# Optimization experiments

Hardware: AMD Instinct MI355X
Metric: run time of the kernel (lower is better)

The kernel has to match this reference:

```python
import jax, jax.numpy as jnp
import numpy as np
from math import sqrt

C = 64        # res_channels
LAYERS = 30
CYCLE = 10
T = 1000
B = 16
L = 32768


def setup_inputs() -> dict:
    key = jax.random.key(0)
    ks = jax.random.split(key, 12)

    def p(k, shape):
        return jax.random.normal(k, shape, dtype=jnp.float32) * 0.05

    # DiffusionEmbedding._build_embedding(T+1): table[s, 2d] = cos(s*10^(4d/63)), table[s,2d+1]=sin(...)
    steps = np.arange(T + 1, dtype=np.float64)[:, None]           # [T+1, 1]
    ang = steps * 10.0 ** (np.arange(64)[None, :] * 4.0 / 63.0)   # [T+1, 64]
    emb_table = jnp.asarray(
        np.stack([np.cos(ang), np.sin(ang)], axis=-1).reshape(T + 1, 128),
        dtype=jnp.float32,
    )

    return {
        "audio": jax.random.normal(ks[0], (B, L), dtype=jnp.float32),
        "diffusion_step": jax.random.randint(ks[1], (B,), 0, T),
        "emb_table": emb_table,                      # [T+1, 128]
        "W1": p(ks[2], (512, 128)), "b1": jnp.zeros((512,), jnp.float32),
        "W2": p(ks[3], (512, 512)), "b2": jnp.zeros((512,), jnp.float32),
        "Win": p(ks[4], (C,)),      "bin_": jnp.zeros((C,), jnp.float32),   # 1x1 conv 1->C
        "diff_W": p(ks[5], (LAYERS, C, 512)),   "diff_b": jnp.zeros((LAYERS, C), jnp.float32),
        "dconv_W": p(ks[6], (LAYERS, 2 * C, C, 3)), "dconv_b": jnp.zeros((LAYERS, 2 * C), jnp.float32),
        "out_W": p(ks[7], (LAYERS, 2 * C, C)),  "out_b": jnp.zeros((LAYERS, 2 * C), jnp.float32),
        "Wo1": p(ks[8], (C, C)),    "bo1": jnp.zeros((C,), jnp.float32),
        "Wo2": p(ks[9], (1, C)),    "bo2": jnp.zeros((1,), jnp.float32),
    }


def _dilated_conv(x, w, d):
    # x: [B, C, L], w: [2C, C, 3], 'same' padding with dilation d
    return jax.lax.conv_general_dilated(
        x, w, window_strides=(1,), padding=[(d, d)], rhs_dilation=(d,),
        dimension_numbers=("NCH", "OIH", "NCH"))


def reference(audio, diffusion_step, emb_table, W1, b1, W2, b2, Win, bin_,
              diff_W, diff_b, dconv_W, dconv_b, out_W, out_b, Wo1, bo1, Wo2, bo2):
    # input projection: Conv1d(1, C, 1) + ReLU
    x = jax.nn.relu(audio[:, None, :] * Win[None, :, None] + bin_[None, :, None])  # [B, C, L]

    t = emb_table[diffusion_step]                  # [B, 128]
    t = jax.nn.silu(t @ W1.T + b1)                 # [B, 512]
    t = jax.nn.silu(t @ W2.T + b2)                 # [B, 512]

    skip = jnp.zeros_like(x)
    for i in range(LAYERS):
        d = 2 ** (i % CYCLE)
        dp = jnp.einsum("bk,ck->bc", t, diff_W[i]) + diff_b[i]          # [B, C]
        y = _dilated_conv(x + dp[:, :, None], dconv_W[i], d)
        y = y + dconv_b[i][None, :, None]                                # [B, 2C, L]
        y = jnp.tanh(y[:, :C]) * jax.nn.sigmoid(y[:, C:])                # gated activation [B, C, L]
        z = jnp.einsum("oc,bcl->bol", out_W[i], y) + out_b[i][None, :, None]  # [B, 2C, L]
        x = (x + z[:, :C]) / sqrt(2.0)
        skip = skip + z[:, C:]

    h = skip / sqrt(float(LAYERS))
    h = jax.nn.relu(jnp.einsum("oc,bcl->bol", Wo1, h) + bo1[None, :, None])
    out = jnp.einsum("oc,bcl->bol", Wo2, h) + bo2[None, :, None]         # [B, 1, L]
    return out[:, 0, :]                                                  # [B, L]
```

## Files before the change

### kernel.cpp

```cpp
#include <hip/hip_runtime.h>
#include <hip/hip_bf16.h>
#include <math.h>
#include <stdint.h>

#define NLAYERS 30
#define BB 16
#define LL 32768
#define SEG 256
#define NT (SEG / 16)

#define SS 16384.0f
#define SSI (1.0f / 16384.0f)

typedef __attribute__((ext_vector_type(8))) short bf16x8;
typedef __attribute__((ext_vector_type(8))) short s16x8;
typedef __attribute__((ext_vector_type(4))) float f32x4;

__device__ inline float bf2f(ushort u) {
    union { uint i; float f; } v; v.i = ((uint)u) << 16; return v.f;
}
__device__ inline ushort f2bf(float f) {
    uint u = __float_as_uint(f);
    return (ushort)((u + 0x7FFFu + ((u >> 16) & 1u)) >> 16);
}

__global__ void emb_kernel(const int* __restrict__ step, const float* __restrict__ emb,
                           const float* __restrict__ W1, const float* __restrict__ b1,
                           const float* __restrict__ W2, const float* __restrict__ b2,
                           float* __restrict__ t_out) {
    int b = blockIdx.x, j = threadIdx.x;
    __shared__ float e[128];
    __shared__ float t1[512];
    int s = step[b];
    if (j < 128) e[j] = emb[s * 128 + j];
    __syncthreads();
    float acc = b1[j];
    const float* w = W1 + j * 128;
    for (int k = 0; k < 128; ++k) acc += w[k] * e[k];
    t1[j] = acc / (1.f + __expf(-acc));
    __syncthreads();
    float acc2 = b2[j];
    const float* w2 = W2 + j * 512;
    for (int k = 0; k < 512; ++k) acc2 += w2[k] * t1[k];
    t_out[b * 512 + j] = acc2 / (1.f + __expf(-acc2));
}

__global__ void dp_kernel(const float* __restrict__ t, const float* __restrict__ diff_W,
                          const float* __restrict__ diff_b, float* __restrict__ dp) {
    int i = blockIdx.x, b = blockIdx.y, c = threadIdx.x;
    __shared__ float ts[512];
    for (int k = c; k < 512; k += 64) ts[k] = t[b * 512 + k];
    __syncthreads();
    const float* w = diff_W + (size_t)(i * 64 + c) * 512;
    float acc = diff_b[i * 64 + c];
    for (int k = 0; k < 512; ++k) acc += w[k] * ts[k];
    dp[(i * BB + b) * 64 + c] = acc;
}

__global__ void prep_w_kernel(const float* __restrict__ dconv_W, ushort* __restrict__ wB,
                              const float* __restrict__ out_W, ushort* __restrict__ oB,
                              const float* __restrict__ Wo1, ushort* __restrict__ Wo1B) {
    int idx = blockIdx.x * 256 + threadIdx.x;
    if (idx < 30 * 8 * 6 * 512) {
        int i = idx / 24576;
        int r = idx % 24576;
        int mt = r / 3072;
        int s = (r / 512) % 6;
        int lane = (r >> 3) & 63;
        int j = r & 7;
        int o = mt * 16 + (lane & 15);
        int tap = s >> 1;
        int c = (s & 1) * 32 + (lane >> 4) * 8 + j;
        wB[idx] = f2bf(dconv_W[((size_t)(i * 128 + o) * 64 + c) * 3 + tap]);
    }
    if (idx < 30 * 8 * 2 * 512) {
        int i = idx / 8192;
        int r = idx % 8192;
        int mt = r / 1024;
        int s = (r / 512) % 2;
        int lane = (r >> 3) & 63;
        int j = r & 7;
        int o = mt * 16 + (lane & 15);
        int c = s * 32 + (lane >> 4) * 8 + j;
        oB[idx] = f2bf(out_W[(size_t)(i * 128 + o) * 64 + c]);
    }
    if (idx < 4 * 2 * 512) {
        int mt = idx / 1024;
        int s = (idx / 512) % 2;
        int lane = (idx >> 3) & 63;
        int j = idx & 7;
        int o = mt * 16 + (lane & 15);
        int c = s * 32 + (lane >> 4) * 8 + j;
        const float hscale = SSI * 0.18257418583505537115f;
        Wo1B[idx] = f2bf(Wo1[o * 64 + c] * hscale);
    }
}

__global__ void bias3_kernel(const float* __restrict__ dp, const float* __restrict__ dconv_W,
                             const float* __restrict__ dconv_b, float* __restrict__ bias3) {
    int i = blockIdx.x, b = blockIdx.y, o = threadIdx.x;
    __shared__ float sdp[64];
    if (o < 64) sdp[o] = dp[(i * BB + b) * 64 + o];
    __syncthreads();
    const float* wrow = dconv_W + (size_t)(i * 128 + o) * 192;
    float f = 0.f, lft = 0.f, rgt = 0.f;
    for (int c = 0; c < 64; ++c) {
        float w0 = wrow[c * 3 + 0], w1 = wrow[c * 3 + 1], w2 = wrow[c * 3 + 2];
        float dv = sdp[c];
        f += dv * (w0 + w1 + w2);
        lft += dv * w0;
        rgt += dv * w2;
    }
    float* dst = bias3 + (size_t)(i * BB + b) * 384;
    dst[o] = f + dconv_b[i * 128 + o];
    dst[128 + o] = lft;
    dst[256 + o] = rgt;
}

__global__ void inproj_kernel(const float* __restrict__ audio, const float* __restrict__ Win,
                              const float* __restrict__ bin_, ushort* __restrict__ x) {
    int idx = blockIdx.x * 256 + threadIdx.x;
    int c8 = idx & 7;
    int l = (idx >> 3) & (LL - 1);
    int b = idx >> 18;
    float a = audio[(size_t)b * LL + l];
    ushort us[8];
    #pragma unroll
    for (int cc = 0; cc < 8; ++cc) {
        int c = c8 * 8 + cc;
        float v = a * Win[c] + bin_[c];
        us[cc] = f2bf(v > 0.f ? v : 0.f);
    }
    ushort4* dst = (ushort4*)(x + ((size_t)b * LL + l) * 64 + c8 * 8);
    dst[0] = make_ushort4(us[0], us[1], us[2], us[3]);
    dst[1] = make_ushort4(us[4], us[5], us[6], us[7]);
}

__global__ __launch_bounds__(256) void layer_fused(
    const ushort* __restrict__ xin, ushort* __restrict__ xout, int16_t* __restrict__ skip,
    const ushort* __restrict__ wB,
    const ushort* __restrict__ oB,
    const float* __restrict__ bias3,
    const float* __restrict__ out_b,
    int d) {
    __shared__ __align__(16) ushort su[2][16][72];

    const int b = blockIdx.y;
    const int seg = blockIdx.x;
    const int tid = threadIdx.x;
    const int lane = tid & 63;
    const int p = tid >> 6;
    const int n = lane & 15;
    const int kg = lane >> 4;
    const int rlo = p * 16 + kg * 4;

    bf16x8 A0[6], A1[6], P0[2], P1[2];
    #pragma unroll
    for (int s = 0; s < 6; ++s) {
        A0[s] = *(const bf16x8*)(wB + ((size_t)(p * 6 + s) * 64 + lane) * 8);
        A1[s] = *(const bf16x8*)(wB + ((size_t)((p + 4) * 6 + s) * 64 + lane) * 8);
    }
    #pragma unroll
    for (int s = 0; s < 2; ++s) {
        P0[s] = *(const bf16x8*)(oB + ((size_t)(p * 2 + s) * 64 + lane) * 8);
        P1[s] = *(const bf16x8*)(oB + ((size_t)((p + 4) * 2 + s) * 64 + lane) * 8);
    }
    const float* bb = bias3 + (size_t)b * 384;
    f32x4 bF_lo = *(const f32x4*)(bb + rlo);
    f32x4 bF_hi = *(const f32x4*)(bb + 64 + rlo);
    f32x4 bL_lo = *(const f32x4*)(bb + 128 + rlo);
    f32x4 bL_hi = *(const f32x4*)(bb + 192 + rlo);
    f32x4 bR_lo = *(const f32x4*)(bb + 256 + rlo);
    f32x4 bR_hi = *(const f32x4*)(bb + 320 + rlo);
    f32x4 obL = *(const f32x4*)(out_b + rlo);
    f32x4 obH = *(const f32x4*)(out_b + 64 + rlo);

    const ushort* xb = xin + (size_t)b * LL * 64;
    ushort* xo = xout + (size_t)b * LL * 64;
    int16_t* sb = skip + (size_t)b * LL * 64;
    const float inv_s2 = 0.70710678118654752440f;

#define LOADB(DST, TT)                                                           \
    {                                                                            \
        const int l0_ = seg * SEG + (TT) * 16;                                   \
        _Pragma("unroll")                                                        \
        for (int tap = 0; tap < 3; ++tap) {                                      \
            int lx = l0_ + n + (tap - 1) * d;                                    \
            bool v = (lx >= 0) && (lx < LL);                                     \
            _Pragma("unroll")                                                    \
            for (int h = 0; h < 2; ++h) {                                        \
                bf16x8 bv = {0, 0, 0, 0, 0, 0, 0, 0};                            \
                if (v) bv = *(const bf16x8*)(xb + (size_t)lx * 64 + h * 32 + kg * 8); \
                DST[tap * 2 + h] = bv;                                           \
            }                                                                    \
        }                                                                        \
    }

#define LOADE(XV, SO, TT)                                                        \
    {                                                                            \
        size_t off_ = (size_t)(seg * SEG + (TT) * 16 + n) * 64 + rlo;            \
        XV = *(const ushort4*)(xb + off_);                                       \
        SO = *(const short4*)(sb + off_);                                        \
    }

#define BODY(TT, BUF, BF, XV, SO)                                                \
    {                                                                            \
        f32x4 accL = {0.f, 0.f, 0.f, 0.f}, accH = {0.f, 0.f, 0.f, 0.f};          \
        _Pragma("unroll")                                                        \
        for (int s = 0; s < 6; ++s) {                                            \
            accL = __builtin_amdgcn_mfma_f32_16x16x32_bf16(A0[s], BF[s], accL, 0, 0, 0); \
            accH = __builtin_amdgcn_mfma_f32_16x16x32_bf16(A1[s], BF[s], accH, 0, 0, 0); \
        }                                                                        \
        const int lx0 = seg * SEG + (TT) * 16 + n;                               \
        float selL = (lx0 < d) ? 1.f : 0.f;                                      \
        float selR = (lx0 >= LL - d) ? 1.f : 0.f;                                \
        ushort4 uq;                                                              \
        _Pragma("unroll")                                                        \
        for (int j = 0; j < 4; ++j) {                                            \
            float lo = accL[j] + bF_lo[j] - selL * bL_lo[j] - selR * bR_lo[j];   \
            float hi = accH[j] + bF_hi[j] - selL * bL_hi[j] - selR * bR_hi[j];   \
            float tv = 1.f - 2.f / (1.f + __expf(2.f * lo));                     \
            float sv = 1.f / (1.f + __expf(-hi));                                \
            ushort q = f2bf(tv * sv);                                            \
            if (j == 0) uq.x = q;                                                \
            if (j == 1) uq.y = q;                                                \
            if (j == 2) uq.z = q;                                                \
            if (j == 3) uq.w = q;                                                \
        }                                                                        \
        *(ushort4*)&su[BUF][n][rlo] = uq;                                        \
        asm volatile("s_waitcnt lgkmcnt(0)" ::: "memory");                       \
        __builtin_amdgcn_s_barrier();                                            \
        asm volatile("" ::: "memory");                                           \
        bf16x8 Bp0 = *(const bf16x8*)&su[BUF][n][kg * 8];                        \
        bf16x8 Bp1 = *(const bf16x8*)&su[BUF][n][32 + kg * 8];                   \
        f32x4 zL = {0.f, 0.f, 0.f, 0.f}, zH = {0.f, 0.f, 0.f, 0.f};              \
        zL = __builtin_amdgcn_mfma_f32_16x16x32_bf16(P0[0], Bp0, zL, 0, 0, 0);   \
        zH = __builtin_amdgcn_mfma_f32_16x16x32_bf16(P1[0], Bp0, zH, 0, 0, 0);   \
        zL = __builtin_amdgcn_mfma_f32_16x16x32_bf16(P0[1], Bp1, zL, 0, 0, 0);   \
        zH = __builtin_amdgcn_mfma_f32_16x16x32_bf16(P1[1], Bp1, zH, 0, 0, 0);   \
        size_t off = (size_t)lx0 * 64 + rlo;                                     \
        ushort4 xn;                                                              \
        xn.x = f2bf((bf2f(XV.x) + zL[0] + obL[0]) * inv_s2);                     \
        xn.y = f2bf((bf2f(XV.y) + zL[1] + obL[1]) * inv_s2);                     \
        xn.z = f2bf((bf2f(XV.z) + zL[2] + obL[2]) * inv_s2);                     \
        xn.w = f2bf((bf2f(XV.w) + zL[3] + obL[3]) * inv_s2);                     \
        *(ushort4*)(xo + off) = xn;                                              \
        short4 sn;                                                               \
        float v;                                                                 \
        v = fminf(fmaxf((float)SO.x * SSI + zH[0] + obH[0], -1.999f), 1.999f);   \
        sn.x = (short)__float2int_rn(v * SS);                                    \
        v = fminf(fmaxf((float)SO.y * SSI + zH[1] + obH[1], -1.999f), 1.999f);   \
        sn.y = (short)__float2int_rn(v * SS);                                    \
        v = fminf(fmaxf((float)SO.z * SSI + zH[2] + obH[2], -1.999f), 1.999f);   \
        sn.z = (short)__float2int_rn(v * SS);                                    \
        v = fminf(fmaxf((float)SO.w * SSI + zH[3] + obH[3], -1.999f), 1.999f);   \
        sn.w = (short)__float2int_rn(v * SS);                                    \
        *(short4*)(sb + off) = sn;                                               \
    }

    bf16x8 FA[6], FB[6];
    ushort4 xvA, xvB;
    short4 soA, soB;
    LOADB(FA, 0)
    LOADE(xvA, soA, 0)
    for (int t = 0; t < NT; t += 2) {
        LOADB(FB, t + 1)
        LOADE(xvB, soB, t + 1)
        BODY(t, 0, FA, xvA, soA)
        const int tn = (t + 2 < NT) ? t + 2 : NT - 2;
        LOADB(FA, tn)
        LOADE(xvA, soA, tn)
        BODY(t + 1, 1, FB, xvB, soB)
    }
#undef LOADB
#undef LOADE
#undef BODY
}

__global__ __launch_bounds__(256) void head_mfma(const int16_t* __restrict__ skip,
                                                 const ushort* __restrict__ Wo1B,
                                                 const float* __restrict__ bo1,
                                                 const float* __restrict__ Wo2,
                                                 const float* __restrict__ bo2,
                                                 float* __restrict__ out) {
    const int b = blockIdx.y;
    const int seg = blockIdx.x;
    const int tid = threadIdx.x;
    const int lane = tid & 63;
    const int w = tid >> 6;
    const int n = lane & 15;
    const int kg = lane >> 4;

    bf16x8 A[4][2];
    #pragma unroll
    for (int mt = 0; mt < 4; ++mt)
        #pragma unroll
        for (int s = 0; s < 2; ++s)
            A[mt][s] = *(const bf16x8*)(Wo1B + ((size_t)(mt * 2 + s) * 64 + lane) * 8);
    f32x4 bo1v[4], wo2v[4];
    #pragma unroll
    for (int mt = 0; mt < 4; ++mt) {
        bo1v[mt] = *(const f32x4*)(bo1 + mt * 16 + kg * 4);
        wo2v[mt] = *(const f32x4*)(Wo2 + mt * 16 + kg * 4);
    }
    const float bo2v = bo2[0];
    const int16_t* sb = skip + (size_t)b * LL * 64;

    for (int t = 0; t < 16; ++t) {
        const int l0 = seg * 1024 + t * 64 + w * 16;
        bf16x8 BH[2], BL[2];
        #pragma unroll
        for (int s = 0; s < 2; ++s) {
            s16x8 v = *(const s16x8*)(sb + (size_t)(l0 + n) * 64 + s * 32 + kg * 8);
            bf16x8 bh, bl;
            #pragma unroll
            for (int e = 0; e < 8; ++e) {
                int sv = (int)v[e];
                int h8 = sv >> 8;
                int l8 = sv - (h8 << 8);
                bh[e] = (short)f2bf((float)h8);
                bl[e] = (short)f2bf((float)l8);
            }
            BH[s] = bh;
            BL[s] = bl;
        }
        f32x4 aH[4], aL[4];
        #pragma unroll
        for (int mt = 0; mt < 4; ++mt) {
            aH[mt] = (f32x4){0.f, 0.f, 0.f, 0.f};
            aL[mt] = (f32x4){0.f, 0.f, 0.f, 0.f};
            #pragma unroll
            for (int s = 0; s < 2; ++s) {
                aH[mt] = __builtin_amdgcn_mfma_f32_16x16x32_bf16(A[mt][s], BH[s], aH[mt], 0, 0, 0);
                aL[mt] = __builtin_amdgcn_mfma_f32_16x16x32_bf16(A[mt][s], BL[s], aL[mt], 0, 0, 0);
            }
        }
        float partial = 0.f;
        #pragma unroll
        for (int mt = 0; mt < 4; ++mt) {
            #pragma unroll
            for (int j = 0; j < 4; ++j) {
                float h = aH[mt][j] * 256.f + aL[mt][j] + bo1v[mt][j];
                partial += (h > 0.f ? h : 0.f) * wo2v[mt][j];
            }
        }
        partial += __shfl_xor(partial, 16, 64);
        partial += __shfl_xor(partial, 32, 64);
        if (kg == 0) out[(size_t)b * LL + l0 + n] = partial + bo2v;
    }
}

extern "C" void kernel_launch(void* const* d_in, const int* in_sizes, int n_in,
                              void* d_out, int out_size, void* d_ws, size_t ws_size,
                              hipStream_t stream) {
    const float* audio = (const float*)d_in[0];
    const int* dstep = (const int*)d_in[1];
    const float* emb = (const float*)d_in[2];
    const float* W1 = (const float*)d_in[3];
    const float* b1 = (const float*)d_in[4];
    const float* W2 = (const float*)d_in[5];
    const float* b2 = (const float*)d_in[6];
    const float* Win = (const float*)d_in[7];
    const float* bin_ = (const float*)d_in[8];
    const float* diff_W = (const float*)d_in[9];
    const float* diff_b = (const float*)d_in[10];
    const float* dconv_W = (const float*)d_in[11];
    const float* dconv_b = (const float*)d_in[12];
    const float* out_W = (const float*)d_in[13];
    const float* out_b = (const float*)d_in[14];
    const float* Wo1 = (const float*)d_in[15];
    const float* bo1 = (const float*)d_in[16];
    const float* Wo2 = (const float*)d_in[17];
    const float* bo2 = (const float*)d_in[18];

    const size_t NACT = (size_t)BB * LL * 64;

    uint8_t* p = (uint8_t*)d_ws;
    ushort* x0 = (ushort*)p;     p += NACT * 2;
    ushort* x1 = (ushort*)p;     p += NACT * 2;
    int16_t* skip = (int16_t*)p; p += NACT * 2;
    float* t = (float*)p;        p += 8192 * 4;
    float* dp = (float*)p;       p += 30720 * 4;
    float* bias3 = (float*)p;    p += 184320 * 4;
    ushort* wB = (ushort*)p;     p += 737280 * 2;
    ushort* oB = (ushort*)p;     p += 245760 * 2;
    ushort* Wo1B = (ushort*)p;   p += 4096 * 2;

    hipMemsetAsync(skip, 0, NACT * 2, stream);
    emb_kernel<<<BB, 512, 0, stream>>>(dstep, emb, W1, b1, W2, b2, t);
    dp_kernel<<<dim3(NLAYERS, BB), 64, 0, stream>>>(t, diff_W, diff_b, dp);
    prep_w_kernel<<<2880, 256, 0, stream>>>(dconv_W, wB, out_W, oB, Wo1, Wo1B);
    bias3_kernel<<<dim3(NLAYERS, BB), 128, 0, stream>>>(dp, dconv_W, dconv_b, bias3);
    inproj_kernel<<<16384, 256, 0, stream>>>(audio, Win, bin_, x0);

    dim3 lgrid(LL / SEG, BB);
    ushort* xin = x0;
    ushort* xout = x1;
    for (int i = 0; i < NLAYERS; ++i) {
        int d = 1 << (i % 10);
        layer_fused<<<lgrid, 256, 0, stream>>>(
            xin, xout, skip, wB + (size_t)i * 24576, oB + (size_t)i * 8192,
            bias3 + (size_t)i * BB * 384, out_b + i * 128, d);
        ushort* tmp = xin; xin = xout; xout = tmp;
    }
    head_mfma<<<dim3(LL / 1024, BB), 256, 0, stream>>>(skip, Wo1B, bo1, Wo2, bo2,
                                                       (float*)d_out);
}
```

Baseline: 4.478 ms.

## Batch two tiles per barrier, use packed bf16 converts, and remap workgroups

The fused layer kernel now runs the first-stage MFMA and gated activation for two 16-column tiles, writes both into a double-buffered LDS slot set, and takes one barrier before both output-projection stages. This halves barrier count per tile pair and lets the next tiles' loads be issued before the barrier. Float-to-bf16 packing uses the hardware v_cvt_pk_bf16_f32 instruction instead of software rounding. The block index is remapped so consecutive workgroups are spread across batch/segments, and launch bounds request 4 waves per SIMD. Loading the E operands later may expose more latency, and the occupancy hint could force register spills.

```diff
diff --git a/kernel.cpp b/kernel.cpp
--- a/kernel.cpp
+++ b/kernel.cpp
@@ -22,6 +22,11 @@
 __device__ inline ushort f2bf(float f) {
     uint u = __float_as_uint(f);
     return (ushort)((u + 0x7FFFu + ((u >> 16) & 1u)) >> 16);
+}
+__device__ inline uint cvtpk(float lo, float hi) {
+    uint r;
+    asm("v_cvt_pk_bf16_f32 %0, %1, %2" : "=v"(r) : "v"(lo), "v"(hi));
+    return r;
 }
 
 __global__ void emb_kernel(const int* __restrict__ step, const float* __restrict__ emb,
@@ -136,17 +141,20 @@
     dst[1] = make_ushort4(us[4], us[5], us[6], us[7]);
 }
 
-__global__ __launch_bounds__(256) void layer_fused(
+__global__ __launch_bounds__(256, 4) void layer_fused(
     const ushort* __restrict__ xin, ushort* __restrict__ xout, int16_t* __restrict__ skip,
     const ushort* __restrict__ wB,
     const ushort* __restrict__ oB,
     const float* __restrict__ bias3,
     const float* __restrict__ out_b,
     int d) {
-    __shared__ __align__(16) ushort su[2][16][72];
-
-    const int b = blockIdx.y;
-    const int seg = blockIdx.x;
+    __shared__ __align__(16) ushort su[2][2][16][72];
+
+    const int nlin = blockIdx.y * gridDim.x + blockIdx.x;
+    const int wgid = (nlin & 7) * 256 + (nlin >> 3);
+    const int seg = wgid & (LL / SEG - 1);
+    const int b = wgid >> 7;
+
     const int tid = threadIdx.x;
     const int lane = tid & 63;
     const int p = tid >> 6;
@@ -203,7 +211,7 @@
         SO = *(const short4*)(sb + off_);                                        \
     }
 
-#define BODY(TT, BUF, BF, XV, SO)                                                \
+#define BODY1(TT, BUF, SLOT, BF)                                                 \
     {                                                                            \
         f32x4 accL = {0.f, 0.f, 0.f, 0.f}, accH = {0.f, 0.f, 0.f, 0.f};          \
         _Pragma("unroll")                                                        \
@@ -214,37 +222,40 @@
         const int lx0 = seg * SEG + (TT) * 16 + n;                               \
         float selL = (lx0 < d) ? 1.f : 0.f;                                      \
         float selR = (lx0 >= LL - d) ? 1.f : 0.f;                                \
-        ushort4 uq;                                                              \
+        float uu[4];                                                             \
         _Pragma("unroll")                                                        \
         for (int j = 0; j < 4; ++j) {                                            \
             float lo = accL[j] + bF_lo[j] - selL * bL_lo[j] - selR * bR_lo[j];   \
             float hi = accH[j] + bF_hi[j] - selL * bL_hi[j] - selR * bR_hi[j];   \
             float tv = 1.f - 2.f / (1.f + __expf(2.f * lo));                     \
             float sv = 1.f / (1.f + __expf(-hi));                                \
-            ushort q = f2bf(tv * sv);                                            \
-            if (j == 0) uq.x = q;                                                \
-            if (j == 1) uq.y = q;                                                \
-            if (j == 2) uq.z = q;                                                \
-            if (j == 3) uq.w = q;                                                \
+            uu[j] = tv * sv;                                                     \
         }                                                                        \
-        *(ushort4*)&su[BUF][n][rlo] = uq;                                        \
-        asm volatile("s_waitcnt lgkmcnt(0)" ::: "memory");                       \
-        __builtin_amdgcn_s_barrier();                                            \
-        asm volatile("" ::: "memory");                                           \
-        bf16x8 Bp0 = *(const bf16x8*)&su[BUF][n][kg * 8];                        \
-        bf16x8 Bp1 = *(const bf16x8*)&su[BUF][n][32 + kg * 8];                   \
+        uint2 uq;                                                                \
+        uq.x = cvtpk(uu[0], uu[1]);                                              \
+        uq.y = cvtpk(uu[2], uu[3]);                                              \
+        *(uint2*)&su[BUF][SLOT][n][rlo] = uq;                                    \
+    }
+
+#define BODY2(TT, BUF, SLOT, XV, SO)                                             \
+    {                                                                            \
+        bf16x8 Bp0 = *(const bf16x8*)&su[BUF][SLOT][n][kg * 8];                  \
+        bf16x8 Bp1 = *(const bf16x8*)&su[BUF][SLOT][n][32 + kg * 8];             \
         f32x4 zL = {0.f, 0.f, 0.f, 0.f}, zH = {0.f, 0.f, 0.f, 0.f};              \
         zL = __builtin_amdgcn_mfma_f32_16x16x32_bf16(P0[0], Bp0, zL, 0, 0, 0);   \
         zH = __builtin_amdgcn_mfma_f32_16x16x32_bf16(P1[0], Bp0, zH, 0, 0, 0);   \
         zL = __builtin_amdgcn_mfma_f32_16x16x32_bf16(P0[1], Bp1, zL, 0, 0, 0);   \
         zH = __builtin_amdgcn_mfma_f32_16x16x32_bf16(P1[1], Bp1, zH, 0, 0, 0);   \
+        const int lx0 = seg * SEG + (TT) * 16 + n;                               \
         size_t off = (size_t)lx0 * 64 + rlo;                                     \
-        ushort4 xn;                                                              \
-        xn.x = f2bf((bf2f(XV.x) + zL[0] + obL[0]) * inv_s2);                     \
-        xn.y = f2bf((bf2f(XV.y) + zL[1] + obL[1]) * inv_s2);                     \
-        xn.z = f2bf((bf2f(XV.z) + zL[2] + obL[2]) * inv_s2);                     \
-        xn.w = f2bf((bf2f(XV.w) + zL[3] + obL[3]) * inv_s2);                     \
-        *(ushort4*)(xo + off) = xn;                                              \
+        float f0 = (bf2f(XV.x) + zL[0] + obL[0]) * inv_s2;                       \
+        float f1 = (bf2f(XV.y) + zL[1] + obL[1]) * inv_s2;                       \
+        float f2 = (bf2f(XV.z) + zL[2] + obL[2]) * inv_s2;                       \
+        float f3 = (bf2f(XV.w) + zL[3] + obL[3]) * inv_s2;                       \
+        uint2 xn;                                                                \
+        xn.x = cvtpk(f0, f1);                                                    \
+        xn.y = cvtpk(f2, f3);                                                    \
+        *(uint2*)(xo + off) = xn;                                                \
         short4 sn;                                                               \
         float v;                                                                 \
         v = fminf(fmaxf((float)SO.x * SSI + zH[0] + obH[0], -1.999f), 1.999f);   \
@@ -262,19 +273,29 @@
     ushort4 xvA, xvB;
     short4 soA, soB;
     LOADB(FA, 0)
+    LOADB(FB, 1)
     LOADE(xvA, soA, 0)
+    LOADE(xvB, soB, 1)
     for (int t = 0; t < NT; t += 2) {
-        LOADB(FB, t + 1)
-        LOADE(xvB, soB, t + 1)
-        BODY(t, 0, FA, xvA, soA)
-        const int tn = (t + 2 < NT) ? t + 2 : NT - 2;
-        LOADB(FA, tn)
-        LOADE(xvA, soA, tn)
-        BODY(t + 1, 1, FB, xvB, soB)
+        const int buf = (t >> 1) & 1;
+        const int ta = (t + 2 < NT) ? t + 2 : t;
+        const int tb = (t + 3 < NT) ? t + 3 : t + 1;
+        BODY1(t, buf, 0, FA)
+        LOADB(FA, ta)
+        BODY1(t + 1, buf, 1, FB)
+        LOADB(FB, tb)
+        asm volatile("s_waitcnt lgkmcnt(0)" ::: "memory");
+        __builtin_amdgcn_s_barrier();
+        asm volatile("" ::: "memory");
+        BODY2(t, buf, 0, xvA, soA)
+        BODY2(t + 1, buf, 1, xvB, soB)
+        LOADE(xvA, soA, ta)
+        LOADE(xvB, soB, tb)
     }
 #undef LOADB
 #undef LOADE
-#undef BODY
+#undef BODY1
+#undef BODY2
 }
 
 __global__ __launch_bounds__(256) void head_mfma(const int16_t* __restrict__ skip,
```

Measured after the change: 12.40 ms. 177% more time.
